# Kernel tuning notes

Measured on AMD Instinct MI355X. Metric: run time of the kernel, lower is better.

Reference implementation:

```python
import jax, jax.numpy as jnp
import numpy as np

N, K, T, NC = 30000, 15, 400, 5
TWO_PI = 2.0 * np.pi
SMOOTH = 0.2  # smoothing_factor default


def setup_inputs() -> dict:
    key = jax.random.key(0)
    ks = jax.random.split(key, 12)
    nw = jax.random.uniform(ks[0], (N, K), jnp.float32) + 1e-3
    lw = jax.random.uniform(ks[1], (N, K), jnp.float32) + 1e-3
    return {
        'time_vector': jnp.arange(T, dtype=jnp.float32),
        'constant_offset': jnp.zeros((N,), jnp.float32),
        'linear_trend': jax.random.normal(ks[2], (N,), jnp.float32) * 0.05,
        'emd_seasonal': jax.random.normal(ks[3], (N, 4, T), jnp.float32),
        'neighbor_indices': jax.random.randint(ks[4], (N, K), 0, N, jnp.int32),
        'neighbor_weights': nw / jnp.sum(nw, axis=1, keepdims=True),
        'local_weights': lw / jnp.sum(lw, axis=1, keepdims=True),
        'residual_amplitudes': jnp.ones((N, NC), jnp.float32) * 3.0,
        'residual_phases': jax.random.uniform(ks[5], (N, NC), jnp.float32) * TWO_PI,
        'residual_periods': jnp.array([25.0, 45.0, 75.0, 150.0, 300.0], jnp.float32),
        'emd_spatial_weights': jnp.ones((N,), jnp.float32) * 0.1,
        'local_spatial_weights': jnp.ones((N,), jnp.float32) * 0.2,
    }


def _smooth(param, idx, w, is_phase):
    # param: [N,C], idx: [N,K], w: [N,K] -> weighted neighbor average blended in
    nbr = param[idx]  # [N,K,C] gather
    if is_phase:
        s = jnp.sum(jnp.sin(nbr) * w[:, :, None], axis=1)
        c = jnp.sum(jnp.cos(nbr) * w[:, :, None], axis=1)
        avg = jnp.arctan2(s, c)
    else:
        avg = jnp.sum(nbr * w[:, :, None], axis=1)
    return (1.0 - SMOOTH) * param + SMOOTH * avg


def reference(time_vector, constant_offset, linear_trend, emd_seasonal,
              neighbor_indices, neighbor_weights, local_weights,
              residual_amplitudes, residual_phases, residual_periods,
              emd_spatial_weights, local_spatial_weights):
    t = time_vector  # [T]
    # linear part: offset + rate * t
    signals = constant_offset[:, None] + linear_trend[:, None] * t[None, :]  # [N,T]

    # --- EMD seasonal with spatial adjustment ---
    emd_signals = jnp.sum(emd_seasonal, axis=1)  # [N,T]
    nbr_sig = emd_signals[neighbor_indices]      # [N,K,T] gather (dominant traffic)
    local_avg = jnp.sum(nbr_sig * local_weights[:, :, None], axis=1)     # [N,T]
    regional_avg = jnp.sum(nbr_sig * neighbor_weights[:, :, None], axis=1)
    ew = jax.nn.sigmoid(emd_spatial_weights)[:, None]   # [N,1]
    lw = jax.nn.sigmoid(local_spatial_weights)[:, None]
    adjusted = (1.0 - ew) * emd_signals + ew * lw * local_avg + ew * (1.0 - lw) * regional_avg
    signals = signals + adjusted

    # --- multi-harmonic residuals with spatially smoothed params ---
    amps = _smooth(residual_amplitudes, neighbor_indices, neighbor_weights, False)  # [N,5]
    phases = _smooth(residual_phases, neighbor_indices, neighbor_weights, True)     # [N,5]
    periods = jnp.clip(residual_periods, 15.0, 350.0)  # [5]
    arg = TWO_PI * t[None, None, :] / periods[None, :, None] + phases[:, :, None]   # [N,5,T]
    residuals = jnp.sum(amps[:, :, None] * jnp.sin(arg), axis=1)                    # [N,T]
    return signals + residuals
```

## Files before the change

kernel.cpp:

```cpp
#include <hip/hip_runtime.h>
#include <math.h>

#define N_ 30000
#define K_ 15
#define T_ 400
#define NC_ 5
#define TQ (T_ / 4)

typedef float f4 __attribute__((ext_vector_type(4)));

static constexpr float TWO_PI_F = 6.283185307179586f;
static constexpr float SMOOTH_F = 0.2f;

__global__ __launch_bounds__(256) void emd_sum_kernel(
    const float* __restrict__ emd, float* __restrict__ out) {
  int g = blockIdx.x * blockDim.x + threadIdx.x;
  if (g >= N_ * TQ) return;
  int n = g / TQ;
  int j = g - n * TQ;
  const f4* row = (const f4*)(emd + (size_t)n * 4 * T_);
  f4 a = __builtin_nontemporal_load(&row[j]);
  f4 b = __builtin_nontemporal_load(&row[j + TQ]);
  f4 c = __builtin_nontemporal_load(&row[j + 2 * TQ]);
  f4 d = __builtin_nontemporal_load(&row[j + 3 * TQ]);
  ((f4*)out)[g] = a + b + c + d;
}

__global__ __launch_bounds__(256) void params_kernel(
    const int* __restrict__ idx, const float* __restrict__ nw,
    const float* __restrict__ amps, const float* __restrict__ phases,
    const float* __restrict__ esw, const float* __restrict__ lsw,
    float* __restrict__ amp_s, float* __restrict__ ph_s,
    float* __restrict__ ew_out, float* __restrict__ lwb_out) {
  int g = blockIdx.x * blockDim.x + threadIdx.x;
  if (g >= N_ * NC_) return;
  int n = g / NC_;
  int c = g - n * NC_;
  float asum = 0.f, ssum = 0.f, csum = 0.f;
#pragma unroll
  for (int k = 0; k < K_; k++) {
    int id = idx[n * K_ + k];
    float w = nw[n * K_ + k];
    asum += w * amps[id * NC_ + c];
    float p = phases[id * NC_ + c];
    ssum += w * __sinf(p);
    csum += w * __cosf(p);
  }
  amp_s[g] = (1.f - SMOOTH_F) * amps[g] + SMOOTH_F * asum;
  ph_s[g] = (1.f - SMOOTH_F) * phases[g] + SMOOTH_F * atan2f(ssum, csum);
  if (c == 0) {
    ew_out[n] = 1.f / (1.f + __expf(-esw[n]));
    lwb_out[n] = 1.f / (1.f + __expf(-lsw[n]));
  }
}

__global__ __launch_bounds__(256) void main_kernel(
    const f4* __restrict__ emd_sig4, const f4* __restrict__ tvec4,
    const int* __restrict__ idx, const float* __restrict__ nw,
    const float* __restrict__ lw, const float* __restrict__ offset,
    const float* __restrict__ trend, const float* __restrict__ ew_arr,
    const float* __restrict__ lwb_arr, const float* __restrict__ amp_s,
    const float* __restrict__ ph_s, const float* __restrict__ periods,
    f4* __restrict__ out4) {
  int g = blockIdx.x * blockDim.x + threadIdx.x;
  if (g >= N_ * TQ) return;
  int n = g / TQ;
  int j = g - n * TQ;
  const int base = n * K_;

  f4 lsum = {0.f, 0.f, 0.f, 0.f};
  f4 rsum = {0.f, 0.f, 0.f, 0.f};
#pragma unroll
  for (int k = 0; k < K_; k++) {
    int id = idx[base + k];
    float wl = lw[base + k];
    float wr = nw[base + k];
    f4 v = emd_sig4[id * TQ + j];
    lsum += wl * v;
    rsum += wr * v;
  }
  f4 own = emd_sig4[n * TQ + j];
  float ew = ew_arr[n];
  float lwb = lwb_arr[n];
  float c_own = 1.f - ew;
  float c_l = ew * lwb;
  float c_r = ew * (1.f - lwb);

  float amp[NC_], ph[NC_], omg[NC_];
#pragma unroll
  for (int c = 0; c < NC_; c++) {
    amp[c] = amp_s[n * NC_ + c];
    ph[c] = ph_s[n * NC_ + c];
    float per = fminf(fmaxf(periods[c], 15.f), 350.f);
    omg[c] = TWO_PI_F / per;
  }

  f4 tf = tvec4[j];
  float off = offset[n];
  float tr = trend[n];

  f4 r = off + tr * tf + c_own * own + c_l * lsum + c_r * rsum;
#pragma unroll
  for (int c = 0; c < NC_; c++) {
    r.x += amp[c] * __sinf(omg[c] * tf.x + ph[c]);
    r.y += amp[c] * __sinf(omg[c] * tf.y + ph[c]);
    r.z += amp[c] * __sinf(omg[c] * tf.z + ph[c]);
    r.w += amp[c] * __sinf(omg[c] * tf.w + ph[c]);
  }
  __builtin_nontemporal_store(r, &out4[g]);
}

__global__ __launch_bounds__(256) void fused_kernel(
    const float* __restrict__ tvec, const float* __restrict__ offset,
    const float* __restrict__ trend, const float* __restrict__ emd,
    const int* __restrict__ idx, const float* __restrict__ nw,
    const float* __restrict__ lw, const float* __restrict__ amps,
    const float* __restrict__ phases, const float* __restrict__ periods,
    const float* __restrict__ esw, const float* __restrict__ lsw,
    float* __restrict__ out) {
  int n = blockIdx.x;
  int tid = threadIdx.x;
  __shared__ int sidx[K_];
  __shared__ float snw[K_], slw[K_];
  __shared__ float samp[NC_], sph[NC_], somega[NC_];
  __shared__ float s_off, s_tr, s_ew, s_lw;
  if (tid < K_) {
    sidx[tid] = idx[n * K_ + tid];
    snw[tid] = nw[n * K_ + tid];
    slw[tid] = lw[n * K_ + tid];
  }
  __syncthreads();
  if (tid < NC_) {
    int c = tid;
    float asum = 0.f, ssum = 0.f, csum = 0.f;
    for (int k = 0; k < K_; k++) {
      int j = sidx[k];
      float w = snw[k];
      asum += w * amps[j * NC_ + c];
      float p = phases[j * NC_ + c];
      ssum += w * __sinf(p);
      csum += w * __cosf(p);
    }
    samp[c] = (1.f - SMOOTH_F) * amps[n * NC_ + c] + SMOOTH_F * asum;
    sph[c] = (1.f - SMOOTH_F) * phases[n * NC_ + c] + SMOOTH_F * atan2f(ssum, csum);
    float per = fminf(fmaxf(periods[c], 15.f), 350.f);
    somega[c] = TWO_PI_F / per;
  } else if (tid == 64) {
    s_off = offset[n];
    s_tr = trend[n];
    s_ew = 1.f / (1.f + __expf(-esw[n]));
    s_lw = 1.f / (1.f + __expf(-lsw[n]));
  }
  __syncthreads();
  float ew = s_ew, lww = s_lw;
  for (int t = tid; t < T_; t += 256) {
    const float* rown = emd + (size_t)n * 4 * T_ + t;
    float own = rown[0] + rown[T_] + rown[2 * T_] + rown[3 * T_];
    float lsum = 0.f, rsum = 0.f;
#pragma unroll
    for (int k = 0; k < K_; k++) {
      const float* rk = emd + (size_t)sidx[k] * 4 * T_ + t;
      float v = rk[0] + rk[T_] + rk[2 * T_] + rk[3 * T_];
      lsum += slw[k] * v;
      rsum += snw[k] * v;
    }
    float adjusted = (1.f - ew) * own + ew * lww * lsum + ew * (1.f - lww) * rsum;
    float tf = tvec[t];
    float res = 0.f;
#pragma unroll
    for (int c = 0; c < NC_; c++) res += samp[c] * __sinf(somega[c] * tf + sph[c]);
    out[(size_t)n * T_ + t] = s_off + s_tr * tf + adjusted + res;
  }
}

extern "C" void kernel_launch(void* const* d_in, const int* in_sizes, int n_in,
                              void* d_out, int out_size, void* d_ws, size_t ws_size,
                              hipStream_t stream) {
  const float* tvec    = (const float*)d_in[0];
  const float* offset  = (const float*)d_in[1];
  const float* trend   = (const float*)d_in[2];
  const float* emd     = (const float*)d_in[3];
  const int*   idx     = (const int*)d_in[4];
  const float* nw      = (const float*)d_in[5];
  const float* lw      = (const float*)d_in[6];
  const float* amps    = (const float*)d_in[7];
  const float* phases  = (const float*)d_in[8];
  const float* periods = (const float*)d_in[9];
  const float* esw     = (const float*)d_in[10];
  const float* lsw     = (const float*)d_in[11];
  float* out = (float*)d_out;

  const size_t emd_sig_bytes = (size_t)N_ * T_ * sizeof(float);
  const size_t par_bytes = (size_t)N_ * NC_ * sizeof(float);
  const size_t n_bytes = (size_t)N_ * sizeof(float);
  const size_t need = emd_sig_bytes + 2 * par_bytes + 2 * n_bytes;

  if (ws_size >= need) {
    char* p = (char*)d_ws;
    float* emd_sig = (float*)p;           p += emd_sig_bytes;
    float* amp_s   = (float*)p;           p += par_bytes;
    float* ph_s    = (float*)p;           p += par_bytes;
    float* ew_arr  = (float*)p;           p += n_bytes;
    float* lwb_arr = (float*)p;           p += n_bytes;

    int totA = N_ * TQ;
    emd_sum_kernel<<<(totA + 255) / 256, 256, 0, stream>>>(emd, emd_sig);
    params_kernel<<<(N_ * NC_ + 255) / 256, 256, 0, stream>>>(
        idx, nw, amps, phases, esw, lsw, amp_s, ph_s, ew_arr, lwb_arr);
    main_kernel<<<(totA + 255) / 256, 256, 0, stream>>>(
        (const f4*)emd_sig, (const f4*)tvec, idx, nw, lw, offset,
        trend, ew_arr, lwb_arr, amp_s, ph_s, periods, (f4*)out);
  } else {
    fused_kernel<<<N_, 256, 0, stream>>>(tvec, offset, trend, emd, idx, nw, lw,
                                         amps, phases, periods, esw, lsw, out);
  }
}
```

Before: 402.3 us.

## Store summed EMD signals in fp16 and fold neighbor weights into one combined weight

The intermediate summed EMD signal is written in half precision, which halves the bytes moved by the gather-heavy main kernel. A new small kernel precomputes one combined per-neighbor weight from the sigmoid blend of the local and regional weights, so the main loop does a single FMA per neighbor. The main kernel now handles 8 time steps per thread with 16-byte fp16 loads. The cost is reduced precision in the intermediate signals, which may cause tolerance errors, plus one extra kernel launch.

```diff
diff --git a/kernel.cpp b/kernel.cpp
--- a/kernel.cpp
+++ b/kernel.cpp
@@ -6,14 +6,17 @@
 #define T_ 400
 #define NC_ 5
 #define TQ (T_ / 4)
+#define TH (T_ / 8)
 
 typedef float f4 __attribute__((ext_vector_type(4)));
+typedef _Float16 h4 __attribute__((ext_vector_type(4)));
+typedef _Float16 h8 __attribute__((ext_vector_type(8)));
 
 static constexpr float TWO_PI_F = 6.283185307179586f;
 static constexpr float SMOOTH_F = 0.2f;
 
 __global__ __launch_bounds__(256) void emd_sum_kernel(
-    const float* __restrict__ emd, float* __restrict__ out) {
+    const float* __restrict__ emd, _Float16* __restrict__ out_h) {
   int g = blockIdx.x * blockDim.x + threadIdx.x;
   if (g >= N_ * TQ) return;
   int n = g / TQ;
@@ -23,15 +26,15 @@
   f4 b = __builtin_nontemporal_load(&row[j + TQ]);
   f4 c = __builtin_nontemporal_load(&row[j + 2 * TQ]);
   f4 d = __builtin_nontemporal_load(&row[j + 3 * TQ]);
-  ((f4*)out)[g] = a + b + c + d;
+  f4 s = a + b + c + d;
+  h4 o = {(_Float16)s.x, (_Float16)s.y, (_Float16)s.z, (_Float16)s.w};
+  ((h4*)out_h)[g] = o;
 }
 
 __global__ __launch_bounds__(256) void params_kernel(
     const int* __restrict__ idx, const float* __restrict__ nw,
     const float* __restrict__ amps, const float* __restrict__ phases,
-    const float* __restrict__ esw, const float* __restrict__ lsw,
-    float* __restrict__ amp_s, float* __restrict__ ph_s,
-    float* __restrict__ ew_out, float* __restrict__ lwb_out) {
+    float* __restrict__ amp_s, float* __restrict__ ph_s) {
   int g = blockIdx.x * blockDim.x + threadIdx.x;
   if (g >= N_ * NC_) return;
   int n = g / NC_;
@@ -48,43 +51,47 @@
   }
   amp_s[g] = (1.f - SMOOTH_F) * amps[g] + SMOOTH_F * asum;
   ph_s[g] = (1.f - SMOOTH_F) * phases[g] + SMOOTH_F * atan2f(ssum, csum);
-  if (c == 0) {
-    ew_out[n] = 1.f / (1.f + __expf(-esw[n]));
-    lwb_out[n] = 1.f / (1.f + __expf(-lsw[n]));
-  }
+}
+
+__global__ __launch_bounds__(256) void cw_kernel(
+    const float* __restrict__ nw, const float* __restrict__ lw,
+    const float* __restrict__ esw, const float* __restrict__ lsw,
+    float* __restrict__ cw, float* __restrict__ c_own) {
+  int g = blockIdx.x * blockDim.x + threadIdx.x;
+  if (g >= N_ * K_) return;
+  int n = g / K_;
+  float ew = 1.f / (1.f + __expf(-esw[n]));
+  float lwb = 1.f / (1.f + __expf(-lsw[n]));
+  cw[g] = ew * (lwb * lw[g] + (1.f - lwb) * nw[g]);
+  if (g - n * K_ == 0) c_own[n] = 1.f - ew;
 }
 
 __global__ __launch_bounds__(256) void main_kernel(
-    const f4* __restrict__ emd_sig4, const f4* __restrict__ tvec4,
-    const int* __restrict__ idx, const float* __restrict__ nw,
-    const float* __restrict__ lw, const float* __restrict__ offset,
-    const float* __restrict__ trend, const float* __restrict__ ew_arr,
-    const float* __restrict__ lwb_arr, const float* __restrict__ amp_s,
+    const h8* __restrict__ emd_h8, const f4* __restrict__ tvec4,
+    const int* __restrict__ idx, const float* __restrict__ cw,
+    const float* __restrict__ c_own, const float* __restrict__ offset,
+    const float* __restrict__ trend, const float* __restrict__ amp_s,
     const float* __restrict__ ph_s, const float* __restrict__ periods,
     f4* __restrict__ out4) {
   int g = blockIdx.x * blockDim.x + threadIdx.x;
-  if (g >= N_ * TQ) return;
-  int n = g / TQ;
-  int j = g - n * TQ;
+  if (g >= N_ * TH) return;
+  int n = g / TH;
+  int j = g - n * TH;
   const int base = n * K_;
 
-  f4 lsum = {0.f, 0.f, 0.f, 0.f};
-  f4 rsum = {0.f, 0.f, 0.f, 0.f};
+  float acc[8] = {0.f, 0.f, 0.f, 0.f, 0.f, 0.f, 0.f, 0.f};
 #pragma unroll
   for (int k = 0; k < K_; k++) {
     int id = idx[base + k];
-    float wl = lw[base + k];
-    float wr = nw[base + k];
-    f4 v = emd_sig4[id * TQ + j];
-    lsum += wl * v;
-    rsum += wr * v;
-  }
-  f4 own = emd_sig4[n * TQ + j];
-  float ew = ew_arr[n];
-  float lwb = lwb_arr[n];
-  float c_own = 1.f - ew;
-  float c_l = ew * lwb;
-  float c_r = ew * (1.f - lwb);
+    float w = cw[base + k];
+    h8 v = emd_h8[(size_t)id * TH + j];
+#pragma unroll
+    for (int i = 0; i < 8; i++) acc[i] += w * (float)v[i];
+  }
+  h8 own = emd_h8[(size_t)n * TH + j];
+  float co = c_own[n];
+  float off = offset[n];
+  float tr = trend[n];
 
   float amp[NC_], ph[NC_], omg[NC_];
 #pragma unroll
@@ -95,19 +102,22 @@
     omg[c] = TWO_PI_F / per;
   }
 
-  f4 tf = tvec4[j];
-  float off = offset[n];
-  float tr = trend[n];
-
-  f4 r = off + tr * tf + c_own * own + c_l * lsum + c_r * rsum;
-#pragma unroll
-  for (int c = 0; c < NC_; c++) {
-    r.x += amp[c] * __sinf(omg[c] * tf.x + ph[c]);
-    r.y += amp[c] * __sinf(omg[c] * tf.y + ph[c]);
-    r.z += amp[c] * __sinf(omg[c] * tf.z + ph[c]);
-    r.w += amp[c] * __sinf(omg[c] * tf.w + ph[c]);
-  }
-  __builtin_nontemporal_store(r, &out4[g]);
+  f4 tf0 = tvec4[2 * j];
+  f4 tf1 = tvec4[2 * j + 1];
+  float t8[8] = {tf0.x, tf0.y, tf0.z, tf0.w, tf1.x, tf1.y, tf1.z, tf1.w};
+
+  float r8[8];
+#pragma unroll
+  for (int i = 0; i < 8; i++) {
+    float r = off + tr * t8[i] + co * (float)own[i] + acc[i];
+#pragma unroll
+    for (int c = 0; c < NC_; c++) r += amp[c] * __sinf(omg[c] * t8[i] + ph[c]);
+    r8[i] = r;
+  }
+  f4 o0 = {r8[0], r8[1], r8[2], r8[3]};
+  f4 o1 = {r8[4], r8[5], r8[6], r8[7]};
+  __builtin_nontemporal_store(o0, &out4[2 * g]);
+  __builtin_nontemporal_store(o1, &out4[2 * g + 1]);
 }
 
 __global__ __launch_bounds__(256) void fused_kernel(
@@ -190,26 +200,28 @@
   const float* lsw     = (const float*)d_in[11];
   float* out = (float*)d_out;
 
-  const size_t emd_sig_bytes = (size_t)N_ * T_ * sizeof(float);
+  const size_t emd_h_bytes = (size_t)N_ * T_ * sizeof(_Float16);
   const size_t par_bytes = (size_t)N_ * NC_ * sizeof(float);
+  const size_t cw_bytes = (size_t)N_ * K_ * sizeof(float);
   const size_t n_bytes = (size_t)N_ * sizeof(float);
-  const size_t need = emd_sig_bytes + 2 * par_bytes + 2 * n_bytes;
+  const size_t need = emd_h_bytes + 2 * par_bytes + cw_bytes + n_bytes;
 
   if (ws_size >= need) {
     char* p = (char*)d_ws;
-    float* emd_sig = (float*)p;           p += emd_sig_bytes;
-    float* amp_s   = (float*)p;           p += par_bytes;
-    float* ph_s    = (float*)p;           p += par_bytes;
-    float* ew_arr  = (float*)p;           p += n_bytes;
-    float* lwb_arr = (float*)p;           p += n_bytes;
-
-    int totA = N_ * TQ;
-    emd_sum_kernel<<<(totA + 255) / 256, 256, 0, stream>>>(emd, emd_sig);
+    _Float16* emd_h = (_Float16*)p;       p += emd_h_bytes;
+    float* amp_s    = (float*)p;          p += par_bytes;
+    float* ph_s     = (float*)p;          p += par_bytes;
+    float* cw       = (float*)p;          p += cw_bytes;
+    float* c_own    = (float*)p;          p += n_bytes;
+
+    emd_sum_kernel<<<(N_ * TQ + 255) / 256, 256, 0, stream>>>(emd, emd_h);
     params_kernel<<<(N_ * NC_ + 255) / 256, 256, 0, stream>>>(
-        idx, nw, amps, phases, esw, lsw, amp_s, ph_s, ew_arr, lwb_arr);
-    main_kernel<<<(totA + 255) / 256, 256, 0, stream>>>(
-        (const f4*)emd_sig, (const f4*)tvec, idx, nw, lw, offset,
-        trend, ew_arr, lwb_arr, amp_s, ph_s, periods, (f4*)out);
+        idx, nw, amps, phases, amp_s, ph_s);
+    cw_kernel<<<(N_ * K_ + 255) / 256, 256, 0, stream>>>(
+        nw, lw, esw, lsw, cw, c_own);
+    main_kernel<<<(N_ * TH + 255) / 256, 256, 0, stream>>>(
+        (const h8*)emd_h, (const f4*)tvec, idx, cw, c_own, offset, trend,
+        amp_s, ph_s, periods, (f4*)out);
   } else {
     fused_kernel<<<N_, 256, 0, stream>>>(tvec, offset, trend, emd, idx, nw, lw,
                                          amps, phases, periods, esw, lsw, out);
```

After: 354.0 us. 12.0% less time.
